# Kernel optimization log

Measured on AMD Instinct MI355X. Metric: run time of the kernel, lower is better.

## Reference

```python
import jax, jax.numpy as jnp
import numpy as np

NC = 4        # num_components
HEADS = 24
DH = 64
D = HEADS * DH  # 1536
EPS = 1e-8


def setup_inputs() -> dict:
    key = jax.random.key(0)
    ks = jax.random.split(key, 7)
    btc, S, E = 4, 4096, 154
    w = lambda k: jax.random.normal(k, (D, D), jnp.float32) * 0.02
    return {
        "hidden_states": jax.random.normal(ks[0], (btc, S, D), jnp.float32),
        "encoder_hidden_states": jax.random.normal(ks[1], (btc, E, D), jnp.float32),
        "temperature": jnp.ones((1,), jnp.float32),
        "Wq": w(ks[2]),
        "Wk": w(ks[3]),
        "Wv": w(ks[4]),
        "Wo": w(ks[5]),
        "bo": jnp.zeros((D,), jnp.float32),
        "pad_length": 154,
    }


def reference(hidden_states, encoder_hidden_states, temperature, Wq, Wk, Wv, Wo, bo, pad_length):
    btc, S, d = hidden_states.shape          # batch*components, latent seq, hidden
    E = encoder_hidden_states.shape[1]       # encoder seq (== pad_length)
    b = btc // NC
    scale = DH ** -0.5
    residual = hidden_states

    def heads(x, L):  # [btc, L, D] -> [btc, H, L, dh]
        return x.reshape(btc, L, HEADS, DH).transpose(0, 2, 1, 3)

    q = heads(hidden_states @ Wq.T, S)
    k = heads(encoder_hidden_states @ Wk.T, E)
    v = heads(encoder_hidden_states @ Wv.T, E)

    # pad tokens are zeros projected through the same k/v weights (no bias -> zeros)
    pad_h = jnp.zeros((btc, pad_length, d), hidden_states.dtype)
    k_pad = heads(pad_h @ Wk.T, pad_length)
    v_pad = heads(pad_h @ Wv.T, pad_length)

    scores = jnp.einsum('bhsd,bhed->bhse', q, k) / (temperature[0] + EPS)
    scores_pad = jnp.einsum('bhsd,bhpd->bhsp', q, k_pad) * scale

    # cross-component softmax over dim 0
    scores = scores.reshape(NC, b, HEADS, S, E)
    scores_pad = scores_pad.reshape(NC, b, HEADS, S, pad_length)
    w = jax.nn.softmax(scores, axis=0)
    w_pad = jax.nn.softmax(scores_pad, axis=0) * (NC / pad_length) * (1.0 - w)

    weights = jnp.concatenate(
        [w.reshape(btc, HEADS, S, E), w_pad.reshape(btc, HEADS, S, pad_length)],
        axis=-1)                              # [btc, H, S, E+pad]
    v_cat = jnp.concatenate([v, v_pad], axis=2)  # [btc, H, E+pad, dh]

    out = jnp.einsum('bhse,bhed->bhsd', weights, v_cat)
    out = out.transpose(0, 2, 1, 3).reshape(btc, S, d)
    out = out @ Wo.T + bo
    return out + residual
```

## Files before the change

kernel.cpp:

```cpp
#include <hip/hip_runtime.h>

typedef __attribute__((ext_vector_type(8))) short short8;
typedef __attribute__((ext_vector_type(4))) float f32x4;
typedef __attribute__((ext_vector_type(4))) unsigned short us4;
typedef __attribute__((ext_vector_type(4))) float float4v;

#define GLB_PTR(p) ((const __attribute__((address_space(1))) void*)(p))
#define LDS_PTR(p) ((__attribute__((address_space(3))) void*)(p))

__device__ __forceinline__ unsigned short f2bf(float f) {
  unsigned int u = __float_as_uint(f);
  u += 0x7FFF + ((u >> 16) & 1);
  return (unsigned short)(u >> 16);
}

__global__ void cvt_all(const float* __restrict__ i0, const float* __restrict__ i1,
                        const float* __restrict__ i2, const float* __restrict__ i3,
                        const float* __restrict__ i4, const float* __restrict__ i5,
                        unsigned short* __restrict__ o0, unsigned short* __restrict__ o1,
                        unsigned short* __restrict__ o2, unsigned short* __restrict__ o3,
                        unsigned short* __restrict__ o4, unsigned short* __restrict__ o5) {
  constexpr int N0 = 16384 * 1536 / 4, N1 = 616 * 1536 / 4, NW = 1536 * 1536 / 4;
  constexpr int TOT = N0 + N1 + 4 * NW;
  int i = blockIdx.x * blockDim.x + threadIdx.x;
  const int stride = gridDim.x * blockDim.x;
  for (; i < TOT; i += stride) {
    const float* in; unsigned short* out; int j = i;
    if (j < N0)              { in = i0; out = o0; }
    else if ((j -= N0) < N1) { in = i1; out = o1; }
    else {
      j -= N1;
      const int t = j / NW; j -= t * NW;
      in  = t == 0 ? i2 : t == 1 ? i3 : t == 2 ? i4 : i5;
      out = t == 0 ? o2 : t == 1 ? o3 : t == 2 ? o4 : o5;
    }
    float4v v = *(const float4v*)(in + (size_t)j * 4);
    us4 o;
    o[0] = f2bf(v[0]); o[1] = f2bf(v[1]); o[2] = f2bf(v[2]); o[3] = f2bf(v[3]);
    *(us4*)(out + (size_t)j * 4) = o;
  }
}

template<int MODE>
__device__ __forceinline__ void gemm_big_body(
    const unsigned short* __restrict__ A,
    const unsigned short* __restrict__ B,
    unsigned short* __restrict__ Cb,
    float* __restrict__ Cf,
    const float* __restrict__ bias,
    const float* __restrict__ resid,
    unsigned short* smem, int bid, int tid) {
  constexpr int K = 1536, N = 1536, BK = 32, NKT = K / BK;
  unsigned short* As = smem;
  unsigned short* Bs = smem + 2 * 8192;

  const int xcd = bid & 7, idx = bid >> 3;
  const int m0 = (xcd * 8 + idx / 12) * 256;
  const int n0 = (idx % 12) * 128;

  const int w = tid >> 6, l = tid & 63, lr = l & 15, lg = l >> 4;
  const int wr = w >> 1, wc = w & 1;
  const int ga = lg ^ (lr & 3);

  const int srow = w * 16 + (l >> 2);
  const int sg = (l & 3) ^ ((l >> 2) & 3);
  const unsigned short* aSrc = A + (size_t)(m0 + srow) * K + sg * 8;
  const unsigned short* bSrc = B + (size_t)(n0 + srow) * K + sg * 8;

  f32x4 acc[4][4] = {};

  auto stage = [&](int buf, int kt) {
    const int k0 = kt * BK;
    unsigned short* AsW = As + buf * 8192 + w * 512;
    unsigned short* BsW = Bs + buf * 4096 + w * 512;
    __builtin_amdgcn_global_load_lds(GLB_PTR(aSrc + k0),                    LDS_PTR(AsW),        16, 0, 0);
    __builtin_amdgcn_global_load_lds(GLB_PTR(aSrc + (size_t)128 * K + k0),  LDS_PTR(AsW + 4096), 16, 0, 0);
    __builtin_amdgcn_global_load_lds(GLB_PTR(bSrc + k0),                    LDS_PTR(BsW),        16, 0, 0);
  };

  auto loadfrags = [&](int buf, short8* af, short8* bfv) {
    const unsigned short* Asb = As + buf * 8192;
    const unsigned short* Bsb = Bs + buf * 4096;
#pragma unroll
    for (int i = 0; i < 4; ++i)
      af[i] = *(const short8*)(Asb + (wr * 64 + i * 16 + lr) * 32 + ga * 8);
#pragma unroll
    for (int j = 0; j < 4; ++j)
      bfv[j] = *(const short8*)(Bsb + (wc * 64 + j * 16 + lr) * 32 + ga * 8);
  };

  auto mfma_all = [&](short8* af, short8* bfv) {
#pragma unroll
    for (int i = 0; i < 4; ++i)
#pragma unroll
      for (int j = 0; j < 4; ++j)
        acc[i][j] = __builtin_amdgcn_mfma_f32_16x16x32_bf16(af[i], bfv[j], acc[i][j], 0, 0, 0);
  };

  stage(0, 0); stage(1, 1);

  for (int kt = 0; kt < NKT; ++kt) {
    if (kt < NKT - 1) asm volatile("s_waitcnt vmcnt(3)" ::: "memory");
    else              asm volatile("s_waitcnt vmcnt(0)" ::: "memory");
    __builtin_amdgcn_s_barrier();
    __builtin_amdgcn_sched_barrier(0);
    short8 af[4], bfv[4];
    loadfrags(kt & 1, af, bfv);
    asm volatile("s_waitcnt lgkmcnt(0)" ::: "memory");
    __builtin_amdgcn_sched_barrier(0);
    __builtin_amdgcn_s_barrier();
    __builtin_amdgcn_sched_barrier(0);
    if (kt + 2 < NKT) stage(kt & 1, kt + 2);
    __builtin_amdgcn_s_setprio(1);
    mfma_all(af, bfv);
    __builtin_amdgcn_s_setprio(0);
  }

#pragma unroll
  for (int i = 0; i < 4; ++i) {
    const int rb = m0 + wr * 64 + i * 16 + lg * 4;
#pragma unroll
    for (int j = 0; j < 4; ++j) {
      const int col = n0 + wc * 64 + j * 16 + lr;
#pragma unroll
      for (int r = 0; r < 4; ++r) {
        size_t o = (size_t)(rb + r) * N + col;
        if (MODE == 0) Cb[o] = f2bf(acc[i][j][r]);
        else           Cf[o] = acc[i][j][r] + bias[col] + resid[o];
      }
    }
  }
}

__device__ __forceinline__ void gemm_kv_body(
    const unsigned short* __restrict__ A,
    const unsigned short* __restrict__ Bk,
    const unsigned short* __restrict__ Bv,
    unsigned short* __restrict__ Ck,
    unsigned short* __restrict__ Vt,
    unsigned short* smem, int by, int tid) {
  constexpr int K = 1536, N = 1536, Mc = 615;
  unsigned short* As = smem;
  unsigned short* Bs = smem + 4096;
  const int bx = by % 5, yy = by / 5;
  const unsigned short* B = yy < 12 ? Bk : Bv;
  const int m0 = bx * 128, n0 = (yy % 12) * 128;
  const bool act = tid < 256;
  const int t = tid;
  const int w = t >> 6, l = t & 63, lr = l & 15, lg = l >> 4;
  const int wr = w >> 1, wc = w & 1;
  const int srow = t >> 2, scol = (t & 3) * 8;

  f32x4 acc[4][4] = {};
  unsigned short* AsW = As + w * 512;
  unsigned short* BsW = Bs + w * 512;
  long ar0 = m0 + srow;       if (ar0 > Mc) ar0 = Mc;
  long ar1 = m0 + srow + 64;  if (ar1 > Mc) ar1 = Mc;

  for (int k0 = 0; k0 < K; k0 += 32) {
    if (act) {
      __builtin_amdgcn_global_load_lds(GLB_PTR(A + ar0 * (long)K + k0 + scol), LDS_PTR(AsW),        16, 0, 0);
      __builtin_amdgcn_global_load_lds(GLB_PTR(A + ar1 * (long)K + k0 + scol), LDS_PTR(AsW + 2048), 16, 0, 0);
      __builtin_amdgcn_global_load_lds(GLB_PTR(B + (long)(n0 + srow) * K + k0 + scol),      LDS_PTR(BsW),        16, 0, 0);
      __builtin_amdgcn_global_load_lds(GLB_PTR(B + (long)(n0 + srow + 64) * K + k0 + scol), LDS_PTR(BsW + 2048), 16, 0, 0);
    }
    __syncthreads();
    if (act) {
      short8 af[4], bfv[4];
#pragma unroll
      for (int i = 0; i < 4; ++i) {
        af[i]  = *(const short8*)(As + (wr * 64 + i * 16 + lr) * 32 + lg * 8);
        bfv[i] = *(const short8*)(Bs + (wc * 64 + i * 16 + lr) * 32 + lg * 8);
      }
#pragma unroll
      for (int i = 0; i < 4; ++i)
#pragma unroll
        for (int j = 0; j < 4; ++j)
          acc[i][j] = __builtin_amdgcn_mfma_f32_16x16x32_bf16(af[i], bfv[j], acc[i][j], 0, 0, 0);
    }
    __syncthreads();
  }

  if (!act) return;
  if (yy < 12) {
#pragma unroll
    for (int i = 0; i < 4; ++i) {
      int rb = m0 + wr * 64 + i * 16 + lg * 4;
#pragma unroll
      for (int j = 0; j < 4; ++j) {
        int col = n0 + wc * 64 + j * 16 + lr;
#pragma unroll
        for (int r = 0; r < 4; ++r)
          Ck[(long)(rb + r) * N + col] = f2bf(acc[i][j][r]);
      }
    }
  } else {
#pragma unroll
    for (int i = 0; i < 4; ++i) {
      int rb = m0 + wr * 64 + i * 16 + lg * 4;
#pragma unroll
      for (int j = 0; j < 4; ++j) {
        int col = n0 + wc * 64 + j * 16 + lr;
        int hh = col >> 6, dd = col & 63;
#pragma unroll
        for (int r = 0; r < 4; ++r) {
          int m = rb + r;
          if (m < 616) {
            int c = (unsigned)m / 154u;
            int e = m - c * 154;
            Vt[((long)((c * 24 + hh) * 64 + dd)) * 160 + e] = f2bf(acc[i][j][r]);
          }
        }
      }
    }
  }
}

__global__ __launch_bounds__(512, 4) void gemm_q_kv(
    const unsigned short* __restrict__ HSb, const unsigned short* __restrict__ Wqb,
    unsigned short* __restrict__ Qb,
    const unsigned short* __restrict__ EHSb, const unsigned short* __restrict__ Wkb,
    const unsigned short* __restrict__ Wvb,
    unsigned short* __restrict__ Ck, unsigned short* __restrict__ Vt) {
  __shared__ unsigned short smem[24576];
  if (blockIdx.x < 768)
    gemm_big_body<0>(HSb, Wqb, Qb, nullptr, nullptr, nullptr, smem, blockIdx.x, threadIdx.x);
  else
    gemm_kv_body(EHSb, Wkb, Wvb, Ck, Vt, smem, blockIdx.x - 768, threadIdx.x);
}

__global__ __launch_bounds__(512, 4) void gemm_o(
    const unsigned short* __restrict__ Ob, const unsigned short* __restrict__ Wob,
    float* __restrict__ Cf, const float* __restrict__ bias, const float* __restrict__ resid) {
  __shared__ unsigned short smem[24576];
  gemm_big_body<1>(Ob, Wob, nullptr, Cf, bias, resid, smem, blockIdx.x, threadIdx.x);
}

__global__ __launch_bounds__(256) void attn_kernel(
    const unsigned short* __restrict__ Qb,
    const unsigned short* __restrict__ Kb,
    const unsigned short* __restrict__ Vt,
    const float* __restrict__ temp,
    unsigned short* __restrict__ Ob) {
  __shared__ unsigned short P[4][4][16][160];
  const int h = blockIdx.y, sb = blockIdx.x;
  const int t = threadIdx.x, w = t >> 6, l = t & 63, lr = l & 15, lg = l >> 4;
  const int s0 = sb * 64 + w * 16;
  const float sc = 1.0f / (temp[0] + 1e-8f);

  short8 qf[4][2];
#pragma unroll
  for (int c = 0; c < 4; ++c)
#pragma unroll
    for (int kt = 0; kt < 2; ++kt)
      qf[c][kt] = *(const short8*)(Qb + (long)(c * 4096 + s0 + lr) * 1536 + h * 64 + kt * 32 + lg * 8);

  short8 kA[4][2], kB[4][2];
  auto loadK = [&](int et, short8 (&k)[4][2]) {
#pragma unroll
    for (int c = 0; c < 4; ++c)
#pragma unroll
      for (int kt = 0; kt < 2; ++kt)
        k[c][kt] = *(const short8*)(Kb + (long)(c * 154 + et * 16 + lr) * 1536 + h * 64 + kt * 32 + lg * 8);
  };

  auto qk_step = [&](int et, short8 (&kc)[4][2], short8 (&kn)[4][2], bool pre) {
    if (pre) loadK(et + 1, kn);
    f32x4 sa[4] = {};
#pragma unroll
    for (int c = 0; c < 4; ++c)
#pragma unroll
      for (int kt = 0; kt < 2; ++kt)
        sa[c] = __builtin_amdgcn_mfma_f32_16x16x32_bf16(kc[c][kt], qf[c][kt], sa[c], 0, 0, 0);
    float wv[4][4];
#pragma unroll
    for (int r = 0; r < 4; ++r) {
      float e0 = __expf(sa[0][r] * sc), e1 = __expf(sa[1][r] * sc);
      float e2 = __expf(sa[2][r] * sc), e3 = __expf(sa[3][r] * sc);
      float inv = 1.0f / (e0 + e1 + e2 + e3);
      wv[0][r] = e0 * inv; wv[1][r] = e1 * inv; wv[2][r] = e2 * inv; wv[3][r] = e3 * inv;
    }
#pragma unroll
    for (int c = 0; c < 4; ++c) {
      us4 pk;
#pragma unroll
      for (int r = 0; r < 4; ++r)
        pk[r] = (et * 16 + lg * 4 + r < 154) ? f2bf(wv[c][r]) : (unsigned short)0;
      *(us4*)&P[w][c][lr][et * 16 + lg * 4] = pk;
    }
  };

  loadK(0, kA);
#pragma unroll
  for (int et = 0; et < 10; et += 2) {
    qk_step(et,     kA, kB, true);
    qk_step(et + 1, kB, kA, et + 1 < 9);
  }
  asm volatile("s_waitcnt lgkmcnt(0)" ::: "memory");
  __builtin_amdgcn_sched_barrier(0);

  short8 vA[4], vB[4];
  auto loadV = [&](int c, int ks, short8 (&v)[4]) {
#pragma unroll
    for (int nt = 0; nt < 4; ++nt)
      v[nt] = *(const short8*)(Vt + (long)((c * 24 + h) * 64 + nt * 16 + lr) * 160 + ks * 32 + lg * 8);
  };

  f32x4 o[4][4] = {};
  loadV(0, 0, vA);
#pragma unroll
  for (int p = 0; p < 10; ++p) {
    const int i0 = 2 * p, i1 = 2 * p + 1;
    const int c0 = i0 / 5, k0 = i0 % 5;
    const int c1 = i1 / 5, k1 = i1 % 5;
    loadV(c1, k1, vB);
    short8 pf0 = *(const short8*)&P[w][c0][lr][k0 * 32 + lg * 8];
#pragma unroll
    for (int nt = 0; nt < 4; ++nt)
      o[c0][nt] = __builtin_amdgcn_mfma_f32_16x16x32_bf16(pf0, vA[nt], o[c0][nt], 0, 0, 0);
    if (p < 9) loadV((i1 + 1) / 5, (i1 + 1) % 5, vA);
    short8 pf1 = *(const short8*)&P[w][c1][lr][k1 * 32 + lg * 8];
#pragma unroll
    for (int nt = 0; nt < 4; ++nt)
      o[c1][nt] = __builtin_amdgcn_mfma_f32_16x16x32_bf16(pf1, vB[nt], o[c1][nt], 0, 0, 0);
  }

  unsigned short* OS = &P[w][0][0][0];
#pragma unroll
  for (int c = 0; c < 4; ++c) {
#pragma unroll
    for (int nt = 0; nt < 4; ++nt)
#pragma unroll
      for (int r = 0; r < 4; ++r)
        OS[(lg * 4 + r) * 64 + nt * 16 + lr] = f2bf(o[c][nt][r]);
    asm volatile("s_waitcnt lgkmcnt(0)" ::: "memory");
    __builtin_amdgcn_sched_barrier(0);
#pragma unroll
    for (int p = 0; p < 2; ++p) {
      const int flat = p * 512 + l * 8;
      const int row = flat >> 6, col = flat & 63;
      short8 v = *(const short8*)(OS + flat);
      *(short8*)(Ob + (long)(c * 4096 + s0 + row) * 1536 + h * 64 + col) = v;
    }
  }
}

extern "C" void kernel_launch(void* const* d_in, const int* in_sizes, int n_in,
                              void* d_out, int out_size, void* d_ws, size_t ws_size,
                              hipStream_t stream) {
  (void)in_sizes; (void)n_in; (void)out_size; (void)ws_size;
  const float* HS  = (const float*)d_in[0];
  const float* EHS = (const float*)d_in[1];
  const float* TMP = (const float*)d_in[2];
  const float* Wq  = (const float*)d_in[3];
  const float* Wk  = (const float*)d_in[4];
  const float* Wv  = (const float*)d_in[5];
  const float* Wo  = (const float*)d_in[6];
  const float* bo  = (const float*)d_in[7];

  char* ws = (char*)d_ws;
  size_t off = 0;
  unsigned short* HSb  = (unsigned short*)(ws + off); off += (size_t)16384 * 1536 * 2;
  unsigned short* Ob   = HSb;
  unsigned short* EHSb = (unsigned short*)(ws + off); off += (size_t)616 * 1536 * 2;
  unsigned short* Wqb  = (unsigned short*)(ws + off); off += (size_t)1536 * 1536 * 2;
  unsigned short* Wkb  = (unsigned short*)(ws + off); off += (size_t)1536 * 1536 * 2;
  unsigned short* Wvb  = (unsigned short*)(ws + off); off += (size_t)1536 * 1536 * 2;
  unsigned short* Wob  = (unsigned short*)(ws + off); off += (size_t)1536 * 1536 * 2;
  unsigned short* Kb   = (unsigned short*)(ws + off); off += (size_t)640 * 1536 * 2;
  unsigned short* Vt   = (unsigned short*)(ws + off); off += (size_t)4 * 24 * 64 * 160 * 2;
  unsigned short* Qb   = (unsigned short*)d_out;

  cvt_all<<<2048, 256, 0, stream>>>(HS, EHS, Wq, Wk, Wv, Wo,
                                    HSb, EHSb, Wqb, Wkb, Wvb, Wob);

  gemm_q_kv<<<888, 512, 0, stream>>>(HSb, Wqb, Qb, EHSb, Wkb, Wvb, Kb, Vt);

  attn_kernel<<<dim3(64, 24), 256, 0, stream>>>(Qb, Kb, Vt, TMP, Ob);

  gemm_o<<<768, 512, 0, stream>>>(Ob, Wob, (float*)d_out, bo, HS);
}
```

Measured before the change: 353.6 us.

## Shrink GEMM tiles with triple-buffered LDS and interleave attention QK with PV

The big GEMMs move from 256x128 to 128x128 tiles, which doubles the grid. They switch to a 3-stage LDS ring so that one barrier per k-step can be dropped. The attention kernel now fuses the QK softmax and PV accumulation per 32-wide key chunk, using a small P buffer in place of materialising all 160 columns first. The goals are better CU load balance, less synchronisation, and lower LDS use in attention. The costs are lower arithmetic intensity per GEMM tile and more frequent waits in attention.

```diff
diff --git a/kernel.cpp b/kernel.cpp
--- a/kernel.cpp
+++ b/kernel.cpp
@@ -52,10 +52,10 @@
     unsigned short* smem, int bid, int tid) {
   constexpr int K = 1536, N = 1536, BK = 32, NKT = K / BK;
   unsigned short* As = smem;
-  unsigned short* Bs = smem + 2 * 8192;
+  unsigned short* Bs = smem + 3 * 4096;
 
   const int xcd = bid & 7, idx = bid >> 3;
-  const int m0 = (xcd * 8 + idx / 12) * 256;
+  const int m0 = (xcd * 16 + idx / 12) * 128;
   const int n0 = (idx % 12) * 128;
 
   const int w = tid >> 6, l = tid & 63, lr = l & 15, lg = l >> 4;
@@ -67,58 +67,49 @@
   const unsigned short* aSrc = A + (size_t)(m0 + srow) * K + sg * 8;
   const unsigned short* bSrc = B + (size_t)(n0 + srow) * K + sg * 8;
 
-  f32x4 acc[4][4] = {};
+  f32x4 acc[2][4] = {};
 
   auto stage = [&](int buf, int kt) {
     const int k0 = kt * BK;
-    unsigned short* AsW = As + buf * 8192 + w * 512;
-    unsigned short* BsW = Bs + buf * 4096 + w * 512;
-    __builtin_amdgcn_global_load_lds(GLB_PTR(aSrc + k0),                    LDS_PTR(AsW),        16, 0, 0);
-    __builtin_amdgcn_global_load_lds(GLB_PTR(aSrc + (size_t)128 * K + k0),  LDS_PTR(AsW + 4096), 16, 0, 0);
-    __builtin_amdgcn_global_load_lds(GLB_PTR(bSrc + k0),                    LDS_PTR(BsW),        16, 0, 0);
+    __builtin_amdgcn_global_load_lds(GLB_PTR(aSrc + k0), LDS_PTR(As + buf * 4096 + w * 512), 16, 0, 0);
+    __builtin_amdgcn_global_load_lds(GLB_PTR(bSrc + k0), LDS_PTR(Bs + buf * 4096 + w * 512), 16, 0, 0);
   };
 
   auto loadfrags = [&](int buf, short8* af, short8* bfv) {
-    const unsigned short* Asb = As + buf * 8192;
+    const unsigned short* Asb = As + buf * 4096;
     const unsigned short* Bsb = Bs + buf * 4096;
 #pragma unroll
-    for (int i = 0; i < 4; ++i)
-      af[i] = *(const short8*)(Asb + (wr * 64 + i * 16 + lr) * 32 + ga * 8);
+    for (int i = 0; i < 2; ++i)
+      af[i] = *(const short8*)(Asb + (wr * 32 + i * 16 + lr) * 32 + ga * 8);
 #pragma unroll
     for (int j = 0; j < 4; ++j)
       bfv[j] = *(const short8*)(Bsb + (wc * 64 + j * 16 + lr) * 32 + ga * 8);
   };
 
-  auto mfma_all = [&](short8* af, short8* bfv) {
-#pragma unroll
-    for (int i = 0; i < 4; ++i)
-#pragma unroll
-      for (int j = 0; j < 4; ++j)
-        acc[i][j] = __builtin_amdgcn_mfma_f32_16x16x32_bf16(af[i], bfv[j], acc[i][j], 0, 0, 0);
-  };
-
   stage(0, 0); stage(1, 1);
 
   for (int kt = 0; kt < NKT; ++kt) {
-    if (kt < NKT - 1) asm volatile("s_waitcnt vmcnt(3)" ::: "memory");
+    if (kt < NKT - 1) asm volatile("s_waitcnt vmcnt(2)" ::: "memory");
     else              asm volatile("s_waitcnt vmcnt(0)" ::: "memory");
     __builtin_amdgcn_s_barrier();
     __builtin_amdgcn_sched_barrier(0);
-    short8 af[4], bfv[4];
-    loadfrags(kt & 1, af, bfv);
+    short8 af[2], bfv[4];
+    loadfrags(kt % 3, af, bfv);
+    if (kt + 2 < NKT) stage((kt + 2) % 3, kt + 2);
     asm volatile("s_waitcnt lgkmcnt(0)" ::: "memory");
     __builtin_amdgcn_sched_barrier(0);
-    __builtin_amdgcn_s_barrier();
-    __builtin_amdgcn_sched_barrier(0);
-    if (kt + 2 < NKT) stage(kt & 1, kt + 2);
     __builtin_amdgcn_s_setprio(1);
-    mfma_all(af, bfv);
+#pragma unroll
+    for (int i = 0; i < 2; ++i)
+#pragma unroll
+      for (int j = 0; j < 4; ++j)
+        acc[i][j] = __builtin_amdgcn_mfma_f32_16x16x32_bf16(af[i], bfv[j], acc[i][j], 0, 0, 0);
     __builtin_amdgcn_s_setprio(0);
   }
 
 #pragma unroll
-  for (int i = 0; i < 4; ++i) {
-    const int rb = m0 + wr * 64 + i * 16 + lg * 4;
+  for (int i = 0; i < 2; ++i) {
+    const int rb = m0 + wr * 32 + i * 16 + lg * 4;
 #pragma unroll
     for (int j = 0; j < 4; ++j) {
       const int col = n0 + wc * 64 + j * 16 + lr;
@@ -223,10 +214,10 @@
     const unsigned short* __restrict__ Wvb,
     unsigned short* __restrict__ Ck, unsigned short* __restrict__ Vt) {
   __shared__ unsigned short smem[24576];
-  if (blockIdx.x < 768)
+  if (blockIdx.x < 1536)
     gemm_big_body<0>(HSb, Wqb, Qb, nullptr, nullptr, nullptr, smem, blockIdx.x, threadIdx.x);
   else
-    gemm_kv_body(EHSb, Wkb, Wvb, Ck, Vt, smem, blockIdx.x - 768, threadIdx.x);
+    gemm_kv_body(EHSb, Wkb, Wvb, Ck, Vt, smem, blockIdx.x - 1536, threadIdx.x);
 }
 
 __global__ __launch_bounds__(512, 4) void gemm_o(
@@ -242,7 +233,7 @@
     const unsigned short* __restrict__ Vt,
     const float* __restrict__ temp,
     unsigned short* __restrict__ Ob) {
-  __shared__ unsigned short P[4][4][16][160];
+  __shared__ unsigned short P2[4][4][16][32];
   const int h = blockIdx.y, sb = blockIdx.x;
   const int t = threadIdx.x, w = t >> 6, l = t & 63, lr = l & 15, lg = l >> 4;
   const int s0 = sb * 64 + w * 16;
@@ -280,24 +271,16 @@
       float inv = 1.0f / (e0 + e1 + e2 + e3);
       wv[0][r] = e0 * inv; wv[1][r] = e1 * inv; wv[2][r] = e2 * inv; wv[3][r] = e3 * inv;
     }
+    const int el = (et & 1) * 16 + lg * 4;
 #pragma unroll
     for (int c = 0; c < 4; ++c) {
       us4 pk;
 #pragma unroll
       for (int r = 0; r < 4; ++r)
         pk[r] = (et * 16 + lg * 4 + r < 154) ? f2bf(wv[c][r]) : (unsigned short)0;
-      *(us4*)&P[w][c][lr][et * 16 + lg * 4] = pk;
-    }
-  };
-
-  loadK(0, kA);
-#pragma unroll
-  for (int et = 0; et < 10; et += 2) {
-    qk_step(et,     kA, kB, true);
-    qk_step(et + 1, kB, kA, et + 1 < 9);
-  }
-  asm volatile("s_waitcnt lgkmcnt(0)" ::: "memory");
-  __builtin_amdgcn_sched_barrier(0);
+      *(us4*)&P2[w][c][lr][el] = pk;
+    }
+  };
 
   short8 vA[4], vB[4];
   auto loadV = [&](int c, int ks, short8 (&v)[4]) {
@@ -307,25 +290,29 @@
   };
 
   f32x4 o[4][4] = {};
+  loadK(0, kA);
   loadV(0, 0, vA);
 #pragma unroll
-  for (int p = 0; p < 10; ++p) {
-    const int i0 = 2 * p, i1 = 2 * p + 1;
-    const int c0 = i0 / 5, k0 = i0 % 5;
-    const int c1 = i1 / 5, k1 = i1 % 5;
-    loadV(c1, k1, vB);
-    short8 pf0 = *(const short8*)&P[w][c0][lr][k0 * 32 + lg * 8];
-#pragma unroll
-    for (int nt = 0; nt < 4; ++nt)
-      o[c0][nt] = __builtin_amdgcn_mfma_f32_16x16x32_bf16(pf0, vA[nt], o[c0][nt], 0, 0, 0);
-    if (p < 9) loadV((i1 + 1) / 5, (i1 + 1) % 5, vA);
-    short8 pf1 = *(const short8*)&P[w][c1][lr][k1 * 32 + lg * 8];
-#pragma unroll
-    for (int nt = 0; nt < 4; ++nt)
-      o[c1][nt] = __builtin_amdgcn_mfma_f32_16x16x32_bf16(pf1, vB[nt], o[c1][nt], 0, 0, 0);
-  }
-
-  unsigned short* OS = &P[w][0][0][0];
+  for (int ks = 0; ks < 5; ++ks) {
+    qk_step(2 * ks,     kA, kB, true);
+    qk_step(2 * ks + 1, kB, kA, ks < 4);
+    asm volatile("s_waitcnt lgkmcnt(0)" ::: "memory");
+    __builtin_amdgcn_sched_barrier(0);
+#pragma unroll
+    for (int c = 0; c < 4; ++c) {
+      if (c == 0)      loadV(1, ks, vB);
+      else if (c == 1) loadV(2, ks, vA);
+      else if (c == 2) loadV(3, ks, vB);
+      else if (ks < 4) loadV(0, ks + 1, vA);
+      short8 pf = *(const short8*)&P2[w][c][lr][lg * 8];
+      short8* vv = (c & 1) ? vB : vA;
+#pragma unroll
+      for (int nt = 0; nt < 4; ++nt)
+        o[c][nt] = __builtin_amdgcn_mfma_f32_16x16x32_bf16(pf, vv[nt], o[c][nt], 0, 0, 0);
+    }
+  }
+
+  unsigned short* OS = &P2[w][0][0][0];
 #pragma unroll
   for (int c = 0; c < 4; ++c) {
 #pragma unroll
@@ -374,9 +361,9 @@
   cvt_all<<<2048, 256, 0, stream>>>(HS, EHS, Wq, Wk, Wv, Wo,
                                     HSb, EHSb, Wqb, Wkb, Wvb, Wob);
 
-  gemm_q_kv<<<888, 512, 0, stream>>>(HSb, Wqb, Qb, EHSb, Wkb, Wvb, Kb, Vt);
+  gemm_q_kv<<<1656, 512, 0, stream>>>(HSb, Wqb, Qb, EHSb, Wkb, Wvb, Kb, Vt);
 
   attn_kernel<<<dim3(64, 24), 256, 0, stream>>>(Qb, Kb, Vt, TMP, Ob);
 
-  gemm_o<<<768, 512, 0, stream>>>(Ob, Wob, (float*)d_out, bo, HS);
-}
+  gemm_o<<<1536, 512, 0, stream>>>(Ob, Wob, (float*)d_out, bo, HS);
+}
```

Result: slower. 386.6 us (+9.3%).
